# Kernel optimization log

Hardware: AMD Instinct MI355X
Metric: run time of the kernel (lower is better)

## Reference

```python
import math
import jax, jax.numpy as jnp
import numpy as np

H = 16  # num_heads
B, L, D = 1, 256, 1024


def setup_inputs() -> dict:
    key = jax.random.key(0)
    ks = jax.random.split(key, 12)
    s = 1.0 / math.sqrt(D)  # keep activations O(1)
    inp = {
        "mu": jax.random.normal(ks[0], (B, L, D), jnp.float32),
        "var": jax.random.uniform(ks[1], (B, L, D), jnp.float32) + 0.1,
    }
    names = ["q_mu", "q_var", "k_mu", "k_var", "v_mu", "v_var", "o_mu", "o_var"]
    for i, n in enumerate(names):
        inp["w" + n] = jax.random.normal(ks[2 + i], (D, D), jnp.float32) * s
        inp["b" + n] = jnp.zeros((D,), jnp.float32)
    return inp


def _split_heads(x):
    b, l, d = x.shape
    return x.reshape(b, l, H, d // H).transpose(0, 2, 1, 3)  # [B,H,L,Dh]


def _combine_heads(x):
    b, h, l, dh = x.shape
    return x.transpose(0, 2, 1, 3).reshape(b, l, h * dh)


def reference(mu, var, wq_mu, bq_mu, wq_var, bq_var, wk_mu, bk_mu, wk_var, bk_var,
              wv_mu, bv_mu, wv_var, bv_var, wo_mu, bo_mu, wo_var, bo_var):
    dk = mu.shape[-1] // H
    Qm = _split_heads(mu @ wq_mu + bq_mu)
    Qv = _split_heads(jax.nn.softplus(var @ wq_var + bq_var))
    Km = _split_heads(mu @ wk_mu + bk_mu)
    Kv = _split_heads(jax.nn.softplus(var @ wk_var + bk_var))
    Vm = _split_heads(mu @ wv_mu + bv_mu)
    Vv = _split_heads(jax.nn.softplus(var @ wv_var + bv_var))

    # per-element Gaussian KL, broadcast to [B,H,Lq,Lk,Dh] (as in the original)
    diff = (Qm[:, :, :, None, :] - Km[:, :, None, :, :]) ** 2
    ratio = Qv[:, :, :, None, :] / Kv[:, :, None, :, :]
    kl = diff / (2.0 * Kv[:, :, None, :, :]) + 0.5 * (ratio - jnp.log(ratio) - 1.0)
    scores = -kl.sum(-1) * (1.0 / math.sqrt(dk))  # [B,H,Lq,Lk]
    attn = jax.nn.softmax(scores, axis=-1)

    out_mu = jnp.einsum("bhqk,bhkd->bhqd", attn, Vm)
    out_var = jnp.einsum("bhqk,bhkd->bhqd", attn ** 2, Vv)

    O_mu = _combine_heads(out_mu)
    O_var = _combine_heads(out_var)
    mu_out = O_mu @ wo_mu + bo_mu
    var_out = jax.nn.softplus(O_var @ wo_var + bo_var)
    return mu_out, var_out
```

## Files before the change

### kernel.cpp

```cpp
#include <hip/hip_runtime.h>
#include <math.h>

typedef __bf16 bf16_t;
typedef bf16_t bf16x4 __attribute__((ext_vector_type(4)));
typedef bf16_t bf16x8 __attribute__((ext_vector_type(8)));
typedef float  f32x4  __attribute__((ext_vector_type(4)));

__device__ __forceinline__ float softplus_f(float x) {
    return (x > 20.f) ? x : log1pf(expf(x));
}

__device__ __forceinline__ float fast_rcp(float x) {
#if __has_builtin(__builtin_amdgcn_rcpf)
    return __builtin_amdgcn_rcpf(x);
#else
    return 1.0f / x;
#endif
}

struct PrepArgs { const float* src[8]; const float* mu; const float* var; };

__global__ __launch_bounds__(256) void prep_kernel(PrepArgs pa, bf16_t* __restrict__ wtbase,
                                                   bf16_t* __restrict__ dmu, bf16_t* __restrict__ dvar) {
    const int t = threadIdx.x;
    if (blockIdx.z == 8) {
        const int gid = (blockIdx.y * 16 + blockIdx.x) * 256 + t;
        const float* s; bf16_t* d; int off;
        if (gid < 32768) { s = pa.mu;  d = dmu;  off = gid * 8; }
        else             { s = pa.var; d = dvar; off = (gid - 32768) * 8; }
        float4 v0 = *(const float4*)(s + off);
        float4 v1 = *(const float4*)(s + off + 4);
        bf16x8 o;
        o[0] = (bf16_t)v0.x; o[1] = (bf16_t)v0.y; o[2] = (bf16_t)v0.z; o[3] = (bf16_t)v0.w;
        o[4] = (bf16_t)v1.x; o[5] = (bf16_t)v1.y; o[6] = (bf16_t)v1.z; o[7] = (bf16_t)v1.w;
        *(bf16x8*)(d + off) = o;
        return;
    }
    const int kt = blockIdx.x, nt = blockIdx.y, wm = blockIdx.z;
    const float* __restrict__ W = pa.src[wm];
    bf16_t* __restrict__ Wt = wtbase + (size_t)wm * 1048576;
    __shared__ bf16_t Ts[64][72];
    const int r0 = t >> 4, c4 = (t & 15) * 4;
#pragma unroll
    for (int rep = 0; rep < 4; ++rep) {
        const int r = r0 + rep * 16;
        const float4 v = *(const float4*)&W[(size_t)(kt * 64 + r) * 1024 + nt * 64 + c4];
        Ts[c4 + 0][r] = (bf16_t)v.x;
        Ts[c4 + 1][r] = (bf16_t)v.y;
        Ts[c4 + 2][r] = (bf16_t)v.z;
        Ts[c4 + 3][r] = (bf16_t)v.w;
    }
    __syncthreads();
#pragma unroll
    for (int rep = 0; rep < 2; ++rep) {
        const int chunk = t + rep * 256;
        const int n = chunk >> 3, kc = (chunk & 7) * 8;
        bf16x8 v = *(const bf16x8*)&Ts[n][kc];
        *(bf16x8*)&Wt[(size_t)(nt * 64 + n) * 1024 + kt * 64 + kc] = v;
    }
}

struct GemmArgs {
    const bf16_t* A[6];
    const bf16_t* Wt[6];
    const float*  bias[6];
    float*        dst[6];
    int           splus[6];
};

__global__ __launch_bounds__(256, 2) void gemm_splitk(GemmArgs args) {
    const int z = blockIdx.z;
    const bf16_t* __restrict__ A    = args.A[z];
    const bf16_t* __restrict__ Wt   = args.Wt[z];
    const float*  __restrict__ bias = args.bias[z];
    float*        __restrict__ dst  = args.dst[z];
    const int sp = args.splus[z];

    const int n_base = blockIdx.x * 64;
    const int m_base = blockIdx.y * 64;

    __shared__ __align__(16) unsigned char smem_raw[73728];
    bf16_t* stage = (bf16_t*)smem_raw;
    float*  Cr    = (float*)smem_raw;

    const int t = threadIdx.x;
    const int lane = t & 63;
    const int w = t >> 6;
    bf16_t* As = stage + w * 9216;
    bf16_t* Bs = As + 4608;

    const int r8 = lane >> 3, kb = lane & 7;
    const int fr = lane & 15, fq = lane >> 4, fk = fq * 8;

    f32x4 acc[4][4] = {};

#pragma unroll
    for (int s = 0; s < 4; ++s) {
        const int k0 = w * 256 + s * 64;
#pragma unroll
        for (int i = 0; i < 8; ++i) {
            const int row = i * 8 + r8;
            bf16x8 av = *(const bf16x8*)&A [(size_t)(m_base + row) * 1024 + k0 + kb * 8];
            bf16x8 bv = *(const bf16x8*)&Wt[(size_t)(n_base + row) * 1024 + k0 + kb * 8];
            *(bf16x8*)&As[row * 72 + kb * 8] = av;
            *(bf16x8*)&Bs[row * 72 + kb * 8] = bv;
        }
#pragma unroll
        for (int kh = 0; kh < 2; ++kh) {
            bf16x8 aF[4], bF[4];
#pragma unroll
            for (int i = 0; i < 4; ++i)
                aF[i] = *(const bf16x8*)&As[(i * 16 + fr) * 72 + kh * 32 + fk];
#pragma unroll
            for (int j = 0; j < 4; ++j)
                bF[j] = *(const bf16x8*)&Bs[(j * 16 + fr) * 72 + kh * 32 + fk];
#pragma unroll
            for (int i = 0; i < 4; ++i)
#pragma unroll
                for (int j = 0; j < 4; ++j)
                    acc[i][j] = __builtin_amdgcn_mfma_f32_16x16x32_bf16(aF[i], bF[j], acc[i][j], 0, 0, 0);
        }
    }

    __syncthreads();
    {
        float* Crw = Cr + w * 4352;
        const int orow = fq * 4;
#pragma unroll
        for (int i = 0; i < 4; ++i)
#pragma unroll
            for (int j = 0; j < 4; ++j)
#pragma unroll
                for (int rr = 0; rr < 4; ++rr)
                    Crw[(i * 16 + orow + rr) * 68 + j * 16 + fr] = acc[i][j][rr];
    }
    __syncthreads();

    const int cc = (t & 15) * 4;
    f32x4 bv4 = *(const f32x4*)&bias[n_base + cc];
#pragma unroll
    for (int i = 0; i < 4; ++i) {
        const int row = (t >> 4) + i * 16;
        f32x4 s0 = *(const f32x4*)&Cr[0 * 4352 + row * 68 + cc];
        f32x4 s1 = *(const f32x4*)&Cr[1 * 4352 + row * 68 + cc];
        f32x4 s2 = *(const f32x4*)&Cr[2 * 4352 + row * 68 + cc];
        f32x4 s3 = *(const f32x4*)&Cr[3 * 4352 + row * 68 + cc];
        f32x4 v = (s0 + s1) + (s2 + s3) + bv4;
        if (sp) {
            v[0] = softplus_f(v[0]); v[1] = softplus_f(v[1]);
            v[2] = softplus_f(v[2]); v[3] = softplus_f(v[3]);
        }
        *(f32x4*)&dst[(size_t)(m_base + row) * 1024 + n_base + cc] = v;
    }
}

__global__ __launch_bounds__(256) void feat_kernel(const float* __restrict__ Km,
                                                   const float* __restrict__ Kv,
                                                   float* __restrict__ G,
                                                   float* __restrict__ cvec) {
    const int h = blockIdx.x, kb = blockIdx.y;
    const int t = threadIdx.x;
    const int kx = t & 63;
    const int dg = t >> 6;
    const int k = kb * 64 + kx;
    const float* kvp = Kv + (size_t)k * 1024 + h * 64 + dg * 16;
    const float* kmp = Km + (size_t)k * 1024 + h * 64 + dg * 16;
    float* gbase = G + (size_t)h * 32768;
    float cp = 0.f;
#pragma unroll
    for (int c = 0; c < 4; ++c) {
        f32x4 kv = *(const f32x4*)(kvp + c * 4);
        f32x4 km = *(const f32x4*)(kmp + c * 4);
#pragma unroll
        for (int e = 0; e < 4; ++e) {
            const int d = dg * 16 + c * 4 + e;
            const float r = 0.5f * fast_rcp(kv[e]);
            gbase[(size_t)d * 256 + k]        = r;
            gbase[(size_t)(64 + d) * 256 + k] = -2.f * km[e] * r;
            cp += km[e] * km[e] * r + 0.5f * __logf(kv[e]);
        }
    }
    __shared__ float red[4][64];
    red[dg][kx] = cp;
    __syncthreads();
    if (dg == 0)
        cvec[h * 256 + k] = red[0][kx] + red[1][kx] + red[2][kx] + red[3][kx];
}

__global__ __launch_bounds__(128) void attn_v3(const float* __restrict__ Qm,
                                               const float* __restrict__ Qv,
                                               const float* __restrict__ G,
                                               const float* __restrict__ cvec,
                                               const float* __restrict__ Vm,
                                               const float* __restrict__ Vv,
                                               bf16_t* __restrict__ Omu,
                                               bf16_t* __restrict__ Ovar) {
    const int bq = blockIdx.x, h = blockIdx.y;
    const int t = threadIdx.x, w = t >> 6, lane = t & 63;
    const int q0 = bq * 8;
    const int fw = w * 4;
    const int qw = q0 + fw;

    __shared__ float Fs[8][128];
    __shared__ float Sc[8][260];

    {
        const int r = t >> 4, c = t & 15;
        const float* qmp = Qm + (size_t)(q0 + r) * 1024 + h * 64 + c * 4;
        const float* qvp = Qv + (size_t)(q0 + r) * 1024 + h * 64 + c * 4;
        f32x4 qm = *(const f32x4*)qmp;
        f32x4 qv = *(const f32x4*)qvp;
        *(f32x4*)&Fs[r][c * 4]      = qm * qm + qv;
        *(f32x4*)&Fs[r][64 + c * 4] = qm;
    }
    __syncthreads();

    f32x4 acc0 = {0.f,0.f,0.f,0.f}, acc1 = acc0, acc2 = acc0, acc3 = acc0;
    const float* gp = G + (size_t)h * 32768 + lane * 4;
#pragma unroll 8
    for (int d = 0; d < 128; ++d) {
        f32x4 g = *(const f32x4*)(gp + (size_t)d * 256);
        acc0 += Fs[fw + 0][d] * g;
        acc1 += Fs[fw + 1][d] * g;
        acc2 += Fs[fw + 2][d] * g;
        acc3 += Fs[fw + 3][d] * g;
    }

    const f32x4 c4 = *(const f32x4*)&cvec[h * 256 + lane * 4];
    f32x4 sr[4];
    sr[0] = (acc0 + c4) * (-0.125f);
    sr[1] = (acc1 + c4) * (-0.125f);
    sr[2] = (acc2 + c4) * (-0.125f);
    sr[3] = (acc3 + c4) * (-0.125f);

#pragma unroll
    for (int r = 0; r < 4; ++r) {
        f32x4 s = sr[r];
        float mloc = fmaxf(fmaxf(s[0], s[1]), fmaxf(s[2], s[3]));
#pragma unroll
        for (int off = 32; off > 0; off >>= 1)
            mloc = fmaxf(mloc, __shfl_xor(mloc, off, 64));
        s[0] = __expf(s[0] - mloc); s[1] = __expf(s[1] - mloc);
        s[2] = __expf(s[2] - mloc); s[3] = __expf(s[3] - mloc);
        float sl = (s[0] + s[1]) + (s[2] + s[3]);
#pragma unroll
        for (int off = 32; off > 0; off >>= 1)
            sl += __shfl_xor(sl, off, 64);
        s *= fast_rcp(sl);
        *(f32x4*)&Sc[fw + r][lane * 4] = s;
    }
    __syncthreads();

    float am[4] = {0.f,0.f,0.f,0.f}, av[4] = {0.f,0.f,0.f,0.f};
    const float* vmp = Vm + h * 64 + lane;
    const float* vvp = Vv + h * 64 + lane;
#pragma unroll 8
    for (int k = 0; k < 256; ++k) {
        const float vm = vmp[(size_t)k * 1024];
        const float vv = vvp[(size_t)k * 1024];
#pragma unroll
        for (int r = 0; r < 4; ++r) {
            const float p = Sc[fw + r][k];
            am[r] += p * vm;
            av[r] += p * p * vv;
        }
    }
#pragma unroll
    for (int r = 0; r < 4; ++r) {
        const size_t ob = (size_t)(qw + r) * 1024 + h * 64 + lane;
        Omu[ob]  = (bf16_t)am[r];
        Ovar[ob] = (bf16_t)av[r];
    }
}

extern "C" void kernel_launch(void* const* d_in, const int* in_sizes, int n_in,
                              void* d_out, int out_size, void* d_ws, size_t ws_size,
                              hipStream_t stream) {
    const float* mu  = (const float*)d_in[0];
    const float* var = (const float*)d_in[1];

    uint8_t* ws = (uint8_t*)d_ws;
    bf16_t* Abf_mu  = (bf16_t*)(ws);
    bf16_t* Abf_var = (bf16_t*)(ws + (512u << 10));
    bf16_t* WtB     = (bf16_t*)(ws + (1u << 20));
    float*  Proj    = (float*)(ws + (17u << 20));
    bf16_t* Obf_mu  = (bf16_t*)(ws + (23u << 20));
    bf16_t* Obf_var = (bf16_t*)(ws + (23u << 20) + (512u << 10));
    float*  G       = (float*)(ws + (24u << 20));
    float*  cvec    = (float*)(ws + (26u << 20));

    PrepArgs pa;
    for (int i = 0; i < 8; ++i) pa.src[i] = (const float*)d_in[2 + 2 * i];
    pa.mu = mu; pa.var = var;
    prep_kernel<<<dim3(16, 16, 9), 256, 0, stream>>>(pa, WtB, Abf_mu, Abf_var);

    GemmArgs g1;
    for (int z = 0; z < 6; ++z) {
        g1.A[z]    = (z & 1) ? Abf_var : Abf_mu;
        g1.Wt[z]   = WtB + (size_t)z * 1048576;
        g1.bias[z] = (const float*)d_in[3 + 2 * z];
        g1.dst[z]  = Proj + (size_t)z * 262144;
        g1.splus[z] = (z & 1);
    }
    gemm_splitk<<<dim3(16, 4, 6), 256, 0, stream>>>(g1);

    feat_kernel<<<dim3(16, 4), 256, 0, stream>>>(Proj + 2 * 262144, Proj + 3 * 262144, G, cvec);

    attn_v3<<<dim3(32, 16), 128, 0, stream>>>(Proj,
                                              Proj + 262144,
                                              G, cvec,
                                              Proj + 4 * 262144,
                                              Proj + 5 * 262144,
                                              Obf_mu, Obf_var);

    GemmArgs g3;
    for (int z = 0; z < 6; ++z) {
        g3.A[z]    = Obf_mu;
        g3.Wt[z]   = WtB + (size_t)6 * 1048576;
        g3.bias[z] = (const float*)d_in[15];
        g3.dst[z]  = (float*)d_out;
        g3.splus[z] = 0;
    }
    g3.A[1]    = Obf_var;
    g3.Wt[1]   = WtB + (size_t)7 * 1048576;
    g3.bias[1] = (const float*)d_in[17];
    g3.dst[1]  = (float*)d_out + 262144;
    g3.splus[1] = 1;
    gemm_splitk<<<dim3(16, 4, 2), 256, 0, stream>>>(g3);
}
```

Measured before the change: 167.3 us.

## Halve GEMM N-tile, register-prefetch K slices, precompute squared probabilities

The split-K GEMM tile width drops from 64 to 32 columns, which doubles the grid and cuts shared memory per block so more blocks can be resident. Global loads for the next K slice are now issued into registers before the MFMAs on the current slice, so load latency overlaps compute. In the attention kernel the squared softmax probabilities are precomputed into a second shared array and read as vectors, which removes per-element multiplies and scalar LDS reads. The price is more redundant reads of the A operand across blocks, higher register pressure from the prefetch buffers, and extra shared memory in the attention kernel.

```diff
diff --git a/kernel.cpp b/kernel.cpp
--- a/kernel.cpp
+++ b/kernel.cpp
@@ -76,75 +76,86 @@
     float*        __restrict__ dst  = args.dst[z];
     const int sp = args.splus[z];
 
-    const int n_base = blockIdx.x * 64;
+    const int n_base = blockIdx.x * 32;
     const int m_base = blockIdx.y * 64;
 
-    __shared__ __align__(16) unsigned char smem_raw[73728];
+    __shared__ __align__(16) unsigned char smem_raw[55296];
     bf16_t* stage = (bf16_t*)smem_raw;
     float*  Cr    = (float*)smem_raw;
 
     const int t = threadIdx.x;
     const int lane = t & 63;
     const int w = t >> 6;
-    bf16_t* As = stage + w * 9216;
+    bf16_t* As = stage + w * 6912;
     bf16_t* Bs = As + 4608;
 
     const int r8 = lane >> 3, kb = lane & 7;
     const int fr = lane & 15, fq = lane >> 4, fk = fq * 8;
 
-    f32x4 acc[4][4] = {};
+    const bf16_t* Ab = A  + (size_t)m_base * 1024 + w * 256 + kb * 8;
+    const bf16_t* Bb = Wt + (size_t)n_base * 1024 + w * 256 + kb * 8;
+
+    f32x4 acc[4][2] = {};
+
+    bf16x8 pa[8], pb[4];
+#pragma unroll
+    for (int i = 0; i < 8; ++i) pa[i] = *(const bf16x8*)(Ab + (size_t)(i * 8 + r8) * 1024);
+#pragma unroll
+    for (int i = 0; i < 4; ++i) pb[i] = *(const bf16x8*)(Bb + (size_t)(i * 8 + r8) * 1024);
 
 #pragma unroll
     for (int s = 0; s < 4; ++s) {
-        const int k0 = w * 256 + s * 64;
-#pragma unroll
-        for (int i = 0; i < 8; ++i) {
-            const int row = i * 8 + r8;
-            bf16x8 av = *(const bf16x8*)&A [(size_t)(m_base + row) * 1024 + k0 + kb * 8];
-            bf16x8 bv = *(const bf16x8*)&Wt[(size_t)(n_base + row) * 1024 + k0 + kb * 8];
-            *(bf16x8*)&As[row * 72 + kb * 8] = av;
-            *(bf16x8*)&Bs[row * 72 + kb * 8] = bv;
+#pragma unroll
+        for (int i = 0; i < 8; ++i) *(bf16x8*)&As[(i * 8 + r8) * 72 + kb * 8] = pa[i];
+#pragma unroll
+        for (int i = 0; i < 4; ++i) *(bf16x8*)&Bs[(i * 8 + r8) * 72 + kb * 8] = pb[i];
+        if (s < 3) {
+            const int off = (s + 1) * 64;
+#pragma unroll
+            for (int i = 0; i < 8; ++i) pa[i] = *(const bf16x8*)(Ab + (size_t)(i * 8 + r8) * 1024 + off);
+#pragma unroll
+            for (int i = 0; i < 4; ++i) pb[i] = *(const bf16x8*)(Bb + (size_t)(i * 8 + r8) * 1024 + off);
         }
 #pragma unroll
         for (int kh = 0; kh < 2; ++kh) {
-            bf16x8 aF[4], bF[4];
+            bf16x8 aF[4], bF[2];
 #pragma unroll
             for (int i = 0; i < 4; ++i)
                 aF[i] = *(const bf16x8*)&As[(i * 16 + fr) * 72 + kh * 32 + fk];
 #pragma unroll
-            for (int j = 0; j < 4; ++j)
+            for (int j = 0; j < 2; ++j)
                 bF[j] = *(const bf16x8*)&Bs[(j * 16 + fr) * 72 + kh * 32 + fk];
 #pragma unroll
             for (int i = 0; i < 4; ++i)
 #pragma unroll
-                for (int j = 0; j < 4; ++j)
+                for (int j = 0; j < 2; ++j)
                     acc[i][j] = __builtin_amdgcn_mfma_f32_16x16x32_bf16(aF[i], bF[j], acc[i][j], 0, 0, 0);
         }
     }
 
     __syncthreads();
     {
-        float* Crw = Cr + w * 4352;
+        float* Crw = Cr + w * 2304;
         const int orow = fq * 4;
 #pragma unroll
         for (int i = 0; i < 4; ++i)
 #pragma unroll
-            for (int j = 0; j < 4; ++j)
+            for (int j = 0; j < 2; ++j)
 #pragma unroll
                 for (int rr = 0; rr < 4; ++rr)
-                    Crw[(i * 16 + orow + rr) * 68 + j * 16 + fr] = acc[i][j][rr];
-    }
-    __syncthreads();
-
-    const int cc = (t & 15) * 4;
+                    Crw[(i * 16 + orow + rr) * 36 + j * 16 + fr] = acc[i][j][rr];
+    }
+    __syncthreads();
+
+    const int cc = (t & 7) * 4;
     f32x4 bv4 = *(const f32x4*)&bias[n_base + cc];
 #pragma unroll
-    for (int i = 0; i < 4; ++i) {
-        const int row = (t >> 4) + i * 16;
-        f32x4 s0 = *(const f32x4*)&Cr[0 * 4352 + row * 68 + cc];
-        f32x4 s1 = *(const f32x4*)&Cr[1 * 4352 + row * 68 + cc];
-        f32x4 s2 = *(const f32x4*)&Cr[2 * 4352 + row * 68 + cc];
-        f32x4 s3 = *(const f32x4*)&Cr[3 * 4352 + row * 68 + cc];
+    for (int it = 0; it < 2; ++it) {
+        const int row = (t >> 3) + it * 32;
+        f32x4 s0 = *(const f32x4*)&Cr[0 * 2304 + row * 36 + cc];
+        f32x4 s1 = *(const f32x4*)&Cr[1 * 2304 + row * 36 + cc];
+        f32x4 s2 = *(const f32x4*)&Cr[2 * 2304 + row * 36 + cc];
+        f32x4 s3 = *(const f32x4*)&Cr[3 * 2304 + row * 36 + cc];
         f32x4 v = (s0 + s1) + (s2 + s3) + bv4;
         if (sp) {
             v[0] = softplus_f(v[0]); v[1] = softplus_f(v[1]);
@@ -187,7 +198,7 @@
         cvec[h * 256 + k] = red[0][kx] + red[1][kx] + red[2][kx] + red[3][kx];
 }
 
-__global__ __launch_bounds__(128) void attn_v3(const float* __restrict__ Qm,
+__global__ __launch_bounds__(128) void attn_v4(const float* __restrict__ Qm,
                                                const float* __restrict__ Qv,
                                                const float* __restrict__ G,
                                                const float* __restrict__ cvec,
@@ -203,6 +214,7 @@
 
     __shared__ float Fs[8][128];
     __shared__ float Sc[8][260];
+    __shared__ float Sc2[8][260];
 
     {
         const int r = t >> 4, c = t & 15;
@@ -247,22 +259,32 @@
         for (int off = 32; off > 0; off >>= 1)
             sl += __shfl_xor(sl, off, 64);
         s *= fast_rcp(sl);
-        *(f32x4*)&Sc[fw + r][lane * 4] = s;
+        *(f32x4*)&Sc[fw + r][lane * 4]  = s;
+        *(f32x4*)&Sc2[fw + r][lane * 4] = s * s;
     }
     __syncthreads();
 
     float am[4] = {0.f,0.f,0.f,0.f}, av[4] = {0.f,0.f,0.f,0.f};
     const float* vmp = Vm + h * 64 + lane;
     const float* vvp = Vv + h * 64 + lane;
-#pragma unroll 8
-    for (int k = 0; k < 256; ++k) {
-        const float vm = vmp[(size_t)k * 1024];
-        const float vv = vvp[(size_t)k * 1024];
-#pragma unroll
-        for (int r = 0; r < 4; ++r) {
-            const float p = Sc[fw + r][k];
-            am[r] += p * vm;
-            av[r] += p * p * vv;
+#pragma unroll 4
+    for (int k4 = 0; k4 < 256; k4 += 4) {
+        f32x4 p0 = *(const f32x4*)&Sc[fw + 0][k4];
+        f32x4 p1 = *(const f32x4*)&Sc[fw + 1][k4];
+        f32x4 p2 = *(const f32x4*)&Sc[fw + 2][k4];
+        f32x4 p3 = *(const f32x4*)&Sc[fw + 3][k4];
+        f32x4 q0v = *(const f32x4*)&Sc2[fw + 0][k4];
+        f32x4 q1v = *(const f32x4*)&Sc2[fw + 1][k4];
+        f32x4 q2v = *(const f32x4*)&Sc2[fw + 2][k4];
+        f32x4 q3v = *(const f32x4*)&Sc2[fw + 3][k4];
+#pragma unroll
+        for (int e = 0; e < 4; ++e) {
+            const float vm = vmp[(size_t)(k4 + e) * 1024];
+            const float vv = vvp[(size_t)(k4 + e) * 1024];
+            am[0] += p0[e] * vm;  av[0] += q0v[e] * vv;
+            am[1] += p1[e] * vm;  av[1] += q1v[e] * vv;
+            am[2] += p2[e] * vm;  av[2] += q2v[e] * vv;
+            am[3] += p3[e] * vm;  av[3] += q3v[e] * vv;
         }
     }
 #pragma unroll
@@ -302,11 +324,11 @@
         g1.dst[z]  = Proj + (size_t)z * 262144;
         g1.splus[z] = (z & 1);
     }
-    gemm_splitk<<<dim3(16, 4, 6), 256, 0, stream>>>(g1);
+    gemm_splitk<<<dim3(32, 4, 6), 256, 0, stream>>>(g1);
 
     feat_kernel<<<dim3(16, 4), 256, 0, stream>>>(Proj + 2 * 262144, Proj + 3 * 262144, G, cvec);
 
-    attn_v3<<<dim3(32, 16), 128, 0, stream>>>(Proj,
+    attn_v4<<<dim3(32, 16), 128, 0, stream>>>(Proj,
                                               Proj + 262144,
                                               G, cvec,
                                               Proj + 4 * 262144,
@@ -326,5 +348,5 @@
     g3.bias[1] = (const float*)d_in[17];
     g3.dst[1]  = (float*)d_out + 262144;
     g3.splus[1] = 1;
-    gemm_splitk<<<dim3(16, 4, 2), 256, 0, stream>>>(g3);
-}
+    gemm_splitk<<<dim3(32, 4, 2), 256, 0, stream>>>(g3);
+}
```

After: 176.0 us. +5.2%, slower.

## Restructure attention kernel: stage G and V in LDS, use bf16 MFMA for PV

Applied to the files above, without the earlier changes.

The attention kernel now processes 16 queries per 256-thread block instead of 8 per 128-thread block. The feature matrix G is staged through LDS in chunks with register prefetch, and V is converted to bf16 in LDS, with those loads interleaved into the score loop. The P·V and P²·Vv products now run on bf16 MFMA instructions, using a hi/lo split of the probabilities to keep precision. This replaces strided scalar global loads of V and the FMA-bound accumulation. In exchange it uses about 105 KB of LDS per block, which limits occupancy, and V is rounded to bf16.

```diff
diff --git a/kernel.cpp b/kernel.cpp
--- a/kernel.cpp
+++ b/kernel.cpp
@@ -187,7 +187,17 @@
         cvec[h * 256 + k] = red[0][kx] + red[1][kx] + red[2][kx] + red[3][kx];
 }
 
-__global__ __launch_bounds__(128) void attn_v3(const float* __restrict__ Qm,
+#define OFF_VM   0
+#define OFF_VV   36864
+#define OFF_GS   73728
+#define OFF_FS   90368
+#define OFF_PHI  73728
+#define OFF_PLO  82176
+#define OFF_P2HI 90624
+#define OFF_P2LO 99072
+#define ATTN_SMEM 107520
+
+__global__ __launch_bounds__(256) void attn_v5(const float* __restrict__ Qm,
                                                const float* __restrict__ Qv,
                                                const float* __restrict__ G,
                                                const float* __restrict__ cvec,
@@ -195,35 +205,91 @@
                                                const float* __restrict__ Vv,
                                                bf16_t* __restrict__ Omu,
                                                bf16_t* __restrict__ Ovar) {
-    const int bq = blockIdx.x, h = blockIdx.y;
+    __shared__ __align__(16) unsigned char smem[ATTN_SMEM];
+    bf16_t* Vsm = (bf16_t*)(smem + OFF_VM);
+    bf16_t* Vsv = (bf16_t*)(smem + OFF_VV);
+    float*  Gs  = (float*)(smem + OFF_GS);
+    float*  Fs  = (float*)(smem + OFF_FS);
+    bf16_t* Phi = (bf16_t*)(smem + OFF_PHI);
+    bf16_t* Plo = (bf16_t*)(smem + OFF_PLO);
+    bf16_t* P2h = (bf16_t*)(smem + OFF_P2HI);
+    bf16_t* P2l = (bf16_t*)(smem + OFF_P2LO);
+
+    const int qt = blockIdx.x, h = blockIdx.y;
     const int t = threadIdx.x, w = t >> 6, lane = t & 63;
-    const int q0 = bq * 8;
+    const int fr = lane & 15, fq = lane >> 4;
     const int fw = w * 4;
-    const int qw = q0 + fw;
-
-    __shared__ float Fs[8][128];
-    __shared__ float Sc[8][260];
 
     {
         const int r = t >> 4, c = t & 15;
-        const float* qmp = Qm + (size_t)(q0 + r) * 1024 + h * 64 + c * 4;
-        const float* qvp = Qv + (size_t)(q0 + r) * 1024 + h * 64 + c * 4;
-        f32x4 qm = *(const f32x4*)qmp;
-        f32x4 qv = *(const f32x4*)qvp;
-        *(f32x4*)&Fs[r][c * 4]      = qm * qm + qv;
-        *(f32x4*)&Fs[r][64 + c * 4] = qm;
+        f32x4 qm = *(const f32x4*)(Qm + (size_t)(qt * 16 + r) * 1024 + h * 64 + c * 4);
+        f32x4 qv = *(const f32x4*)(Qv + (size_t)(qt * 16 + r) * 1024 + h * 64 + c * 4);
+        *(f32x4*)&Fs[r * 132 + c * 4]      = qm * qm + qv;
+        *(f32x4*)&Fs[r * 132 + 64 + c * 4] = qm;
+    }
+
+    const float* gsrc = G + (size_t)h * 32768 + (size_t)(t >> 4) * 256 + (t & 15) * 16;
+    {
+        f32x4 g0 = *(const f32x4*)(gsrc);
+        f32x4 g1 = *(const f32x4*)(gsrc + 4);
+        f32x4 g2 = *(const f32x4*)(gsrc + 8);
+        f32x4 g3 = *(const f32x4*)(gsrc + 12);
+        float* gd = &Gs[(t >> 4) * 260 + (t & 15) * 16];
+        *(f32x4*)(gd)      = g0;
+        *(f32x4*)(gd + 4)  = g1;
+        *(f32x4*)(gd + 8)  = g2;
+        *(f32x4*)(gd + 12) = g3;
     }
     __syncthreads();
 
     f32x4 acc0 = {0.f,0.f,0.f,0.f}, acc1 = acc0, acc2 = acc0, acc3 = acc0;
-    const float* gp = G + (size_t)h * 32768 + lane * 4;
-#pragma unroll 8
-    for (int d = 0; d < 128; ++d) {
-        f32x4 g = *(const f32x4*)(gp + (size_t)d * 256);
-        acc0 += Fs[fw + 0][d] * g;
-        acc1 += Fs[fw + 1][d] * g;
-        acc2 += Fs[fw + 2][d] * g;
-        acc3 += Fs[fw + 3][d] * g;
+    const int vk = t >> 2, vpart = t & 3;
+
+    for (int c = 0; c < 8; ++c) {
+        f32x4 g0, g1, g2, g3;
+        if (c < 7) {
+            const float* s = gsrc + (size_t)(c + 1) * 4096;
+            g0 = *(const f32x4*)(s);
+            g1 = *(const f32x4*)(s + 4);
+            g2 = *(const f32x4*)(s + 8);
+            g3 = *(const f32x4*)(s + 12);
+        }
+        const int rep = c & 3;
+        const int kkv = vk + rep * 64;
+        const float* vsrc = ((c >> 2) ? Vv : Vm) + (size_t)kkv * 1024 + h * 64 + vpart * 16;
+        f32x4 v0 = *(const f32x4*)(vsrc);
+        f32x4 v1 = *(const f32x4*)(vsrc + 4);
+        f32x4 v2 = *(const f32x4*)(vsrc + 8);
+        f32x4 v3 = *(const f32x4*)(vsrc + 12);
+
+#pragma unroll
+        for (int dl = 0; dl < 16; ++dl) {
+            f32x4 g = *(const f32x4*)&Gs[dl * 260 + lane * 4];
+            const int d = c * 16 + dl;
+            acc0 += Fs[(fw + 0) * 132 + d] * g;
+            acc1 += Fs[(fw + 1) * 132 + d] * g;
+            acc2 += Fs[(fw + 2) * 132 + d] * g;
+            acc3 += Fs[(fw + 3) * 132 + d] * g;
+        }
+        __syncthreads();
+        {
+            bf16_t* vdst = ((c >> 2) ? Vsv : Vsm) + kkv * 72 + vpart * 16;
+            bf16x8 o0, o1;
+            o0[0]=(bf16_t)v0[0]; o0[1]=(bf16_t)v0[1]; o0[2]=(bf16_t)v0[2]; o0[3]=(bf16_t)v0[3];
+            o0[4]=(bf16_t)v1[0]; o0[5]=(bf16_t)v1[1]; o0[6]=(bf16_t)v1[2]; o0[7]=(bf16_t)v1[3];
+            o1[0]=(bf16_t)v2[0]; o1[1]=(bf16_t)v2[1]; o1[2]=(bf16_t)v2[2]; o1[3]=(bf16_t)v2[3];
+            o1[4]=(bf16_t)v3[0]; o1[5]=(bf16_t)v3[1]; o1[6]=(bf16_t)v3[2]; o1[7]=(bf16_t)v3[3];
+            *(bf16x8*)(vdst)     = o0;
+            *(bf16x8*)(vdst + 8) = o1;
+        }
+        if (c < 7) {
+            float* gd = &Gs[(t >> 4) * 260 + (t & 15) * 16];
+            *(f32x4*)(gd)      = g0;
+            *(f32x4*)(gd + 4)  = g1;
+            *(f32x4*)(gd + 8)  = g2;
+            *(f32x4*)(gd + 12) = g3;
+        }
+        __syncthreads();
     }
 
     const f32x4 c4 = *(const f32x4*)&cvec[h * 256 + lane * 4];
@@ -246,30 +312,56 @@
 #pragma unroll
         for (int off = 32; off > 0; off >>= 1)
             sl += __shfl_xor(sl, off, 64);
-        s *= fast_rcp(sl);
-        *(f32x4*)&Sc[fw + r][lane * 4] = s;
-    }
-    __syncthreads();
-
-    float am[4] = {0.f,0.f,0.f,0.f}, av[4] = {0.f,0.f,0.f,0.f};
-    const float* vmp = Vm + h * 64 + lane;
-    const float* vvp = Vv + h * 64 + lane;
-#pragma unroll 8
-    for (int k = 0; k < 256; ++k) {
-        const float vm = vmp[(size_t)k * 1024];
-        const float vv = vvp[(size_t)k * 1024];
-#pragma unroll
-        for (int r = 0; r < 4; ++r) {
-            const float p = Sc[fw + r][k];
-            am[r] += p * vm;
-            av[r] += p * p * vv;
-        }
-    }
+        sr[r] = s * fast_rcp(sl);
+    }
+
 #pragma unroll
     for (int r = 0; r < 4; ++r) {
-        const size_t ob = (size_t)(qw + r) * 1024 + h * 64 + lane;
-        Omu[ob]  = (bf16_t)am[r];
-        Ovar[ob] = (bf16_t)av[r];
+        bf16x4 phi, plo, p2hi, p2lo;
+#pragma unroll
+        for (int e = 0; e < 4; ++e) {
+            const float p = sr[r][e];
+            const bf16_t hb = (bf16_t)p;
+            phi[e] = hb; plo[e] = (bf16_t)(p - (float)hb);
+            const float p2 = p * p;
+            const bf16_t h2 = (bf16_t)p2;
+            p2hi[e] = h2; p2lo[e] = (bf16_t)(p2 - (float)h2);
+        }
+        const int row = fw + r;
+        *(bf16x4*)&Phi[row * 264 + lane * 4] = phi;
+        *(bf16x4*)&Plo[row * 264 + lane * 4] = plo;
+        *(bf16x4*)&P2h[row * 264 + lane * 4] = p2hi;
+        *(bf16x4*)&P2l[row * 264 + lane * 4] = p2lo;
+    }
+    __syncthreads();
+
+    f32x4 accm = {0.f,0.f,0.f,0.f}, accv = {0.f,0.f,0.f,0.f};
+#pragma unroll
+    for (int k0 = 0; k0 < 256; k0 += 32) {
+        const int ka = k0 + fq * 8;
+        bf16x8 ahi = *(const bf16x8*)&Phi[fr * 264 + ka];
+        bf16x8 alo = *(const bf16x8*)&Plo[fr * 264 + ka];
+        bf16x8 a2h = *(const bf16x8*)&P2h[fr * 264 + ka];
+        bf16x8 a2l = *(const bf16x8*)&P2l[fr * 264 + ka];
+        bf16x8 bm, bv;
+#pragma unroll
+        for (int j = 0; j < 8; ++j) {
+            const int kk = ka + j;
+            bm[j] = Vsm[kk * 72 + w * 16 + fr];
+            bv[j] = Vsv[kk * 72 + w * 16 + fr];
+        }
+        accm = __builtin_amdgcn_mfma_f32_16x16x32_bf16(ahi, bm, accm, 0, 0, 0);
+        accm = __builtin_amdgcn_mfma_f32_16x16x32_bf16(alo, bm, accm, 0, 0, 0);
+        accv = __builtin_amdgcn_mfma_f32_16x16x32_bf16(a2h, bv, accv, 0, 0, 0);
+        accv = __builtin_amdgcn_mfma_f32_16x16x32_bf16(a2l, bv, accv, 0, 0, 0);
+    }
+
+#pragma unroll
+    for (int reg = 0; reg < 4; ++reg) {
+        const int qg = qt * 16 + fq * 4 + reg;
+        const size_t ob = (size_t)qg * 1024 + h * 64 + w * 16 + fr;
+        Omu[ob]  = (bf16_t)accm[reg];
+        Ovar[ob] = (bf16_t)accv[reg];
     }
 }
 
@@ -306,7 +398,7 @@
 
     feat_kernel<<<dim3(16, 4), 256, 0, stream>>>(Proj + 2 * 262144, Proj + 3 * 262144, G, cvec);
 
-    attn_v3<<<dim3(32, 16), 128, 0, stream>>>(Proj,
+    attn_v5<<<dim3(16, 16), 256, 0, stream>>>(Proj,
                                               Proj + 262144,
                                               G, cvec,
                                               Proj + 4 * 262144,
```

After: 153.0 us. 8.5% less time.
